# Kernel optimization log

Measured on AMD Instinct MI355X. Metric: run time of the kernel, lower is better.

Reference implementation:

```python
import jax, jax.numpy as jnp
import numpy as np

I_SIZE = 2048
O_SIZE = 2048
NUM_DOMAINS = 20
B, T = 16, 2048


def setup_inputs() -> dict:
    key = jax.random.key(0)
    k_x, k_w, k_d = jax.random.split(key, 3)
    x = jax.random.normal(k_x, (B, T, I_SIZE), dtype=jnp.float32)
    domain_id = jax.random.randint(k_d, (B,), 0, NUM_DOMAINS)
    # xavier_uniform over [num_domains, O*I]
    limit = float(np.sqrt(6.0 / (NUM_DOMAINS + O_SIZE * I_SIZE)))
    fc_weight = jax.random.uniform(k_w, (NUM_DOMAINS, O_SIZE * I_SIZE), dtype=jnp.float32, minval=-limit, maxval=limit)
    bias_weight = jnp.zeros((NUM_DOMAINS, O_SIZE), dtype=jnp.float32)
    return {"x": x, "domain_id": domain_id, "fc_weight": fc_weight, "bias_weight": bias_weight}


def reference(x, domain_id, fc_weight, bias_weight):
    # Gather per-sample weights: [B, I, O] (flat row reshaped as (I, O))
    W = fc_weight[domain_id].reshape(-1, I_SIZE, O_SIZE)
    b = bias_weight[domain_id]  # [B, O]
    # y = x @ W + b : [B, T, O]
    y = jnp.einsum('bti,bio->bto', x, W) + b[:, None, :]
    return y
```

## Files before the change

kernel.cpp:

```cpp
#include <hip/hip_runtime.h>
#include <hip/hip_bf16.h>
#include <stdint.h>

typedef __attribute__((ext_vector_type(4))) float  f32x4;
typedef __attribute__((ext_vector_type(8))) short  s16x8;
typedef __attribute__((ext_vector_type(4))) short  s16x4;

constexpr int I_SZ = 2048;
constexpr int O_SZ = 2048;
constexpr int T_SZ = 2048;
constexpr int B_MAX = 16;

constexpr size_t XT_ELEMS = (size_t)B_MAX * T_SZ * I_SZ;
constexpr size_t WT_ELEMS = (size_t)B_MAX * I_SZ * O_SZ;
constexpr size_t WS_NEEDED = (XT_ELEMS + WT_ELEMS) * sizeof(short);

__device__ __forceinline__ short f2bf(float f) {
    __hip_bfloat16 h = __float2bfloat16(f);
    return *reinterpret_cast<short*>(&h);
}

__device__ __forceinline__ void gload_lds16(const void* g, void* l) {
    __builtin_amdgcn_global_load_lds(
        (const __attribute__((address_space(1))) unsigned int*)g,
        (__attribute__((address_space(3))) unsigned int*)l, 16, 0, 0);
}

__global__ __launch_bounds__(256) void convA(const float* __restrict__ x,
                                             short* __restrict__ xt) {
    const int c = blockIdx.x * 256 + threadIdx.x;
    const int l  = c & 63;
    const int mi = (c >> 6) & 7;
    const int kt = (c >> 9) & 63;
    const int rest = c >> 15;
    const int mt = rest & 15, bz = rest >> 4;
    const int lr = l & 15, hi = l >> 4;
    const int m = mt * 128 + mi * 16 + lr;
    const float* src = x + ((size_t)(bz * T_SZ + m)) * I_SZ + kt * 32 + 4 * hi;
    f32x4 a = *reinterpret_cast<const f32x4*>(src);
    f32x4 b = *reinterpret_cast<const f32x4*>(src + 16);
    s16x8 h = { f2bf(a[0]), f2bf(a[1]), f2bf(a[2]), f2bf(a[3]),
                f2bf(b[0]), f2bf(b[1]), f2bf(b[2]), f2bf(b[3]) };
    *reinterpret_cast<s16x8*>(xt + (size_t)c * 8) = h;
}

__global__ __launch_bounds__(256) void convB(const float* __restrict__ fcw,
                                             const int* __restrict__ dom_id,
                                             short* __restrict__ wt) {
    const int c = blockIdx.x * 256 + threadIdx.x;
    const int l  = c & 63;
    const int ni = (c >> 6) & 7;
    const int kt = (c >> 9) & 63;
    const int rest = c >> 15;
    const int nt = rest & 15, bz = rest >> 4;
    const int lr = l & 15, hi = l >> 4;
    const int n = nt * 128 + ni * 16 + lr;
    const int dom = dom_id[bz];
    const float* src = fcw + (size_t)dom * ((size_t)I_SZ * O_SZ)
                           + (size_t)(kt * 32 + 4 * hi) * O_SZ + n;
    short h[8];
    #pragma unroll
    for (int j = 0; j < 4; ++j) {
        h[j]     = f2bf(src[(size_t)j * O_SZ]);
        h[4 + j] = f2bf(src[(size_t)(16 + j) * O_SZ]);
    }
    *reinterpret_cast<s16x8*>(wt + (size_t)c * 8) =
        *reinterpret_cast<s16x8*>(h);
}

__global__ __launch_bounds__(256, 2) void gemm_128x256(
        const short* __restrict__ xt, const short* __restrict__ wt,
        const float* __restrict__ bw, const int* __restrict__ dom_id,
        float* __restrict__ out) {
    __shared__ short As[3][8192];

    const int bid = blockIdx.x;
    const int swz = (bid & 7) * 256 + (bid >> 3);
    const int bz = swz >> 7;
    const int mb = (swz >> 3) & 15;
    const int nb = swz & 7;

    const int t = threadIdx.x;
    const int wv = t >> 6, l = t & 63;
    const int lr = l & 15, hi = l >> 4;
    const int nti  = wv >> 1;
    const int bsub = (wv & 1) * 4;

    const short* Abase = xt + (size_t)(bz * 16 + mb) * 64 * 4096;
    const short* Bp = wt + (size_t)((bz * 16 + nb * 2 + nti) * 64) * 4096
                         + bsub * 512 + l * 8;

    auto stageA = [&](int buf, int T) {
        #pragma unroll
        for (int r = 0; r < 4; ++r)
            gload_lds16(Abase + (size_t)(2 * T) * 4096 + r * 2048 + t * 8,
                        &As[buf][r * 2048 + t * 8]);
    };

    f32x4 acc[8][4] = {};

    stageA(0, 0);

    for (int T = 0; T < 32; ++T) {
        const int d = T % 3;

        s16x8 bq0[4], bq1[4];
        {
            const short* b0 = Bp + (size_t)(2 * T) * 4096;
            #pragma unroll
            for (int g = 0; g < 4; ++g)
                bq0[g] = *reinterpret_cast<const s16x8*>(b0 + g * 512);
            #pragma unroll
            for (int g = 0; g < 4; ++g)
                bq1[g] = *reinterpret_cast<const s16x8*>(b0 + 4096 + g * 512);
        }

        const int nT = (T + 1 < 32) ? T + 1 : 31;
        stageA((T + 1) % 3, nT);

        asm volatile("s_waitcnt vmcnt(4)" ::: "memory");
        asm volatile("s_barrier" ::: "memory");

        s16x8 af[8];
        #pragma unroll
        for (int f = 0; f < 8; ++f)
            af[f] = *reinterpret_cast<const s16x8*>(&As[d][f * 512 + l * 8]);
        __builtin_amdgcn_s_setprio(1);
        #pragma unroll
        for (int f = 0; f < 8; ++f)
            #pragma unroll
            for (int g = 0; g < 4; ++g)
                acc[f][g] = __builtin_amdgcn_mfma_f32_16x16x32_bf16(
                                af[f], bq0[g], acc[f][g], 0, 0, 0);
        __builtin_amdgcn_s_setprio(0);

        #pragma unroll
        for (int f = 0; f < 8; ++f)
            af[f] = *reinterpret_cast<const s16x8*>(&As[d][4096 + f * 512 + l * 8]);
        __builtin_amdgcn_s_setprio(1);
        #pragma unroll
        for (int f = 0; f < 8; ++f)
            #pragma unroll
            for (int g = 0; g < 4; ++g)
                acc[f][g] = __builtin_amdgcn_mfma_f32_16x16x32_bf16(
                                af[f], bq1[g], acc[f][g], 0, 0, 0);
        __builtin_amdgcn_s_setprio(0);
    }

    asm volatile("s_waitcnt vmcnt(0)" ::: "memory");

    const int dom = dom_id[bz];
    const int col0 = nb * 256 + wv * 64;
    float bias[4];
    #pragma unroll
    for (int g = 0; g < 4; ++g)
        bias[g] = bw[dom * O_SZ + col0 + g * 16 + lr];

    const size_t obase = ((size_t)bz * T_SZ + mb * 128) * O_SZ + col0;
    #pragma unroll
    for (int f = 0; f < 8; ++f) {
        #pragma unroll
        for (int r = 0; r < 4; ++r) {
            const int row = f * 16 + hi * 4 + r;
            float* orow = out + obase + (size_t)row * O_SZ;
            #pragma unroll
            for (int g = 0; g < 4; ++g)
                orow[g * 16 + lr] = acc[f][g][r] + bias[g];
        }
    }
}

constexpr int BM = 128, BN = 128, BK = 32;
constexpr int LDK = 40;
constexpr int NKT = I_SZ / BK;

__global__ __launch_bounds__(256) void dal_gemm(
    const float* __restrict__ x, const int* __restrict__ dom_id,
    const float* __restrict__ fcw, const float* __restrict__ bw,
    float* __restrict__ out)
{
    __shared__ short As[2][BM * LDK];
    __shared__ short Bs[2][BN * LDK];
    const int bz = blockIdx.z;
    const int m0 = blockIdx.y * BM, n0 = blockIdx.x * BN;
    const int dom = dom_id[bz];
    const float* Ag = x + ((size_t)bz * T_SZ + m0) * I_SZ;
    const float* Wg = fcw + (size_t)dom * ((size_t)I_SZ * O_SZ) + n0;
    const int t = threadIdx.x;
    const int am = t >> 3, ac = (t & 7) << 2;
    const int bk = (t >> 5) << 2, bn = (t & 31) << 2;
    const int wv = t >> 6, lane = t & 63;
    const int wr = (wv >> 1) << 6, wc = (wv & 1) << 6;
    const int hi = lane >> 4, lr = lane & 15;
    f32x4 acc[4][4] = {};
    f32x4 ra[4], rb[4];
    auto load_tile = [&](int kb) {
        #pragma unroll
        for (int p = 0; p < 4; ++p)
            ra[p] = *reinterpret_cast<const f32x4*>(Ag + (size_t)(am + 32 * p) * I_SZ + kb + ac);
        #pragma unroll
        for (int r = 0; r < 4; ++r)
            rb[r] = *reinterpret_cast<const f32x4*>(Wg + (size_t)(kb + bk + r) * O_SZ + bn);
    };
    auto store_tile = [&](int buf) {
        #pragma unroll
        for (int p = 0; p < 4; ++p) {
            s16x4 h = { f2bf(ra[p][0]), f2bf(ra[p][1]), f2bf(ra[p][2]), f2bf(ra[p][3]) };
            *reinterpret_cast<s16x4*>(&As[buf][(am + 32 * p) * LDK + ac]) = h;
        }
        #pragma unroll
        for (int i = 0; i < 4; ++i) {
            s16x4 h = { f2bf(rb[0][i]), f2bf(rb[1][i]), f2bf(rb[2][i]), f2bf(rb[3][i]) };
            *reinterpret_cast<s16x4*>(&Bs[buf][(bn + i) * LDK + bk]) = h;
        }
    };
    load_tile(0);
    store_tile(0);
    __syncthreads();
    for (int kt = 0; kt < NKT; ++kt) {
        const int cur = kt & 1;
        if (kt + 1 < NKT) load_tile((kt + 1) * BK);
        s16x8 af[4], bfr[4];
        #pragma unroll
        for (int im = 0; im < 4; ++im) {
            const short* p = &As[cur][(wr + im * 16 + lr) * LDK + 4 * hi];
            s16x4 lo = *reinterpret_cast<const s16x4*>(p);
            s16x4 hh = *reinterpret_cast<const s16x4*>(p + 16);
            af[im] = __builtin_shufflevector(lo, hh, 0, 1, 2, 3, 4, 5, 6, 7);
        }
        #pragma unroll
        for (int in = 0; in < 4; ++in) {
            const short* p = &Bs[cur][(wc + in * 16 + lr) * LDK + 4 * hi];
            s16x4 lo = *reinterpret_cast<const s16x4*>(p);
            s16x4 hh = *reinterpret_cast<const s16x4*>(p + 16);
            bfr[in] = __builtin_shufflevector(lo, hh, 0, 1, 2, 3, 4, 5, 6, 7);
        }
        #pragma unroll
        for (int im = 0; im < 4; ++im)
            #pragma unroll
            for (int in = 0; in < 4; ++in)
                acc[im][in] = __builtin_amdgcn_mfma_f32_16x16x32_bf16(
                                  af[im], bfr[in], acc[im][in], 0, 0, 0);
        if (kt + 1 < NKT) store_tile(cur ^ 1);
        __syncthreads();
    }
    float bias[4];
    #pragma unroll
    for (int in = 0; in < 4; ++in)
        bias[in] = bw[dom * O_SZ + n0 + wc + in * 16 + lr];
    const size_t obase = ((size_t)bz * T_SZ + m0) * O_SZ + n0;
    #pragma unroll
    for (int im = 0; im < 4; ++im) {
        #pragma unroll
        for (int r = 0; r < 4; ++r) {
            const int row = wr + im * 16 + hi * 4 + r;
            float* orow = out + obase + (size_t)row * O_SZ;
            #pragma unroll
            for (int in = 0; in < 4; ++in)
                orow[wc + in * 16 + lr] = acc[im][in][r] + bias[in];
        }
    }
}

extern "C" void kernel_launch(void* const* d_in, const int* in_sizes, int n_in,
                              void* d_out, int out_size, void* d_ws, size_t ws_size,
                              hipStream_t stream) {
    const float* x   = (const float*)d_in[0];
    const int*   dom = (const int*)d_in[1];
    const float* fcw = (const float*)d_in[2];
    const float* bw  = (const float*)d_in[3];
    float* out = (float*)d_out;
    const int B = in_sizes[1];

    if (ws_size >= WS_NEEDED && B == B_MAX) {
        short* xt = (short*)d_ws;
        short* wt = xt + XT_ELEMS;
        const int chunks = B * 16 * 64 * 512;
        convA<<<chunks / 256, 256, 0, stream>>>(x, xt);
        convB<<<chunks / 256, 256, 0, stream>>>(fcw, dom, wt);
        gemm_128x256<<<dim3(2048), dim3(256), 0, stream>>>(xt, wt, bw, dom, out);
    } else {
        dim3 grid(O_SZ / BN, T_SZ / BM, B);
        dal_gemm<<<grid, dim3(256), 0, stream>>>(x, dom, fcw, bw, out);
    }
}
```

Baseline: 404.0 us.

## Switch GEMM to 32x32x16 MFMA with repacked operands and deeper prefetch

Replaces the 16x16x32 bf16 MFMA tiles with 32x32x16 MFMA and changes the convA/convB pre-packing layouts to match the new fragment shape. It also restructures the main loop so B fragments for the next step load right after each half-phase and A tiles are staged two steps ahead in the triple buffer. The aim is fewer MFMA issues and LDS reads per FLOP, plus more overlap of global loads with compute. The epilogue is rewritten for the 32x32 accumulator layout, and the wait-count logic now depends on the new load ordering.

New measurement: 454.1 us. 12.4% more time.

```diff
diff --git a/kernel.cpp b/kernel.cpp
--- a/kernel.cpp
+++ b/kernel.cpp
@@ -2,9 +2,10 @@
 #include <hip/hip_bf16.h>
 #include <stdint.h>
 
-typedef __attribute__((ext_vector_type(4))) float  f32x4;
-typedef __attribute__((ext_vector_type(8))) short  s16x8;
-typedef __attribute__((ext_vector_type(4))) short  s16x4;
+typedef __attribute__((ext_vector_type(4)))  float f32x4;
+typedef __attribute__((ext_vector_type(16))) float f32x16;
+typedef __attribute__((ext_vector_type(8)))  short s16x8;
+typedef __attribute__((ext_vector_type(4)))  short s16x4;
 
 constexpr int I_SZ = 2048;
 constexpr int O_SZ = 2048;
@@ -29,16 +30,16 @@
 __global__ __launch_bounds__(256) void convA(const float* __restrict__ x,
                                              short* __restrict__ xt) {
     const int c = blockIdx.x * 256 + threadIdx.x;
-    const int l  = c & 63;
-    const int mi = (c >> 6) & 7;
-    const int kt = (c >> 9) & 63;
+    const int l   = c & 63;
+    const int sub = (c >> 6) & 3;
+    const int kt  = (c >> 8) & 127;
     const int rest = c >> 15;
     const int mt = rest & 15, bz = rest >> 4;
-    const int lr = l & 15, hi = l >> 4;
-    const int m = mt * 128 + mi * 16 + lr;
-    const float* src = x + ((size_t)(bz * T_SZ + m)) * I_SZ + kt * 32 + 4 * hi;
+    const int m = mt * 128 + sub * 32 + (l & 31);
+    const int kbase = kt * 16 + 4 * (l >> 5);
+    const float* src = x + ((size_t)(bz * T_SZ + m)) * I_SZ + kbase;
     f32x4 a = *reinterpret_cast<const f32x4*>(src);
-    f32x4 b = *reinterpret_cast<const f32x4*>(src + 16);
+    f32x4 b = *reinterpret_cast<const f32x4*>(src + 8);
     s16x8 h = { f2bf(a[0]), f2bf(a[1]), f2bf(a[2]), f2bf(a[3]),
                 f2bf(b[0]), f2bf(b[1]), f2bf(b[2]), f2bf(b[3]) };
     *reinterpret_cast<s16x8*>(xt + (size_t)c * 8) = h;
@@ -48,21 +49,21 @@
                                              const int* __restrict__ dom_id,
                                              short* __restrict__ wt) {
     const int c = blockIdx.x * 256 + threadIdx.x;
-    const int l  = c & 63;
-    const int ni = (c >> 6) & 7;
-    const int kt = (c >> 9) & 63;
+    const int l   = c & 63;
+    const int sub = (c >> 6) & 3;
+    const int kt  = (c >> 8) & 127;
     const int rest = c >> 15;
     const int nt = rest & 15, bz = rest >> 4;
-    const int lr = l & 15, hi = l >> 4;
-    const int n = nt * 128 + ni * 16 + lr;
+    const int n = nt * 128 + sub * 32 + (l & 31);
+    const int kbase = kt * 16 + 4 * (l >> 5);
     const int dom = dom_id[bz];
     const float* src = fcw + (size_t)dom * ((size_t)I_SZ * O_SZ)
-                           + (size_t)(kt * 32 + 4 * hi) * O_SZ + n;
+                           + (size_t)kbase * O_SZ + n;
     short h[8];
     #pragma unroll
     for (int j = 0; j < 4; ++j) {
         h[j]     = f2bf(src[(size_t)j * O_SZ]);
-        h[4 + j] = f2bf(src[(size_t)(16 + j) * O_SZ]);
+        h[4 + j] = f2bf(src[(size_t)(8 + j) * O_SZ]);
     }
     *reinterpret_cast<s16x8*>(wt + (size_t)c * 8) =
         *reinterpret_cast<s16x8*>(h);
@@ -82,90 +83,101 @@
 
     const int t = threadIdx.x;
     const int wv = t >> 6, l = t & 63;
-    const int lr = l & 15, hi = l >> 4;
-    const int nti  = wv >> 1;
-    const int bsub = (wv & 1) * 4;
-
-    const short* Abase = xt + (size_t)(bz * 16 + mb) * 64 * 4096;
-    const short* Bp = wt + (size_t)((bz * 16 + nb * 2 + nti) * 64) * 4096
+    const int lc = l & 31, lh = l >> 5;
+    const int nt128 = nb * 2 + (wv >> 1);
+    const int bsub  = 2 * (wv & 1);
+
+    const short* Abase = xt + (size_t)(bz * 16 + mb) * 262144;
+    const short* Bp = wt + (size_t)(bz * 16 + nt128) * 262144
                          + bsub * 512 + l * 8;
 
     auto stageA = [&](int buf, int T) {
         #pragma unroll
         for (int r = 0; r < 4; ++r)
-            gload_lds16(Abase + (size_t)(2 * T) * 4096 + r * 2048 + t * 8,
+            gload_lds16(Abase + (size_t)(4 * T + r) * 2048 + t * 8,
                         &As[buf][r * 2048 + t * 8]);
     };
 
-    f32x4 acc[8][4] = {};
+    f32x16 acc[4][2] = {};
+    s16x8 bqS0[4], bqS1[4];
+
+    auto loadS0 = [&](int T) {
+        #pragma unroll
+        for (int rr = 0; rr < 2; ++rr)
+            #pragma unroll
+            for (int g = 0; g < 2; ++g)
+                bqS0[rr * 2 + g] = *reinterpret_cast<const s16x8*>(
+                    Bp + (size_t)(4 * T + rr) * 2048 + g * 512);
+    };
+    auto loadS1 = [&](int T) {
+        #pragma unroll
+        for (int rr = 0; rr < 2; ++rr)
+            #pragma unroll
+            for (int g = 0; g < 2; ++g)
+                bqS1[rr * 2 + g] = *reinterpret_cast<const s16x8*>(
+                    Bp + (size_t)(4 * T + 2 + rr) * 2048 + g * 512);
+    };
+
+    auto phase = [&](int d, int r0, const s16x8* bq) {
+        #pragma unroll
+        for (int rr = 0; rr < 2; ++rr) {
+            const int r = r0 + rr;
+            s16x8 af[4];
+            #pragma unroll
+            for (int s = 0; s < 4; ++s)
+                af[s] = *reinterpret_cast<const s16x8*>(
+                            &As[d][r * 2048 + s * 512 + l * 8]);
+            __builtin_amdgcn_s_setprio(1);
+            #pragma unroll
+            for (int s = 0; s < 4; ++s)
+                #pragma unroll
+                for (int g = 0; g < 2; ++g)
+                    acc[s][g] = __builtin_amdgcn_mfma_f32_32x32x16_bf16(
+                                    af[s], bq[rr * 2 + g], acc[s][g], 0, 0, 0);
+            __builtin_amdgcn_s_setprio(0);
+        }
+    };
 
     stageA(0, 0);
+    loadS0(0);
+    loadS1(0);
+    stageA(1, 1);
 
     for (int T = 0; T < 32; ++T) {
         const int d = T % 3;
-
-        s16x8 bq0[4], bq1[4];
-        {
-            const short* b0 = Bp + (size_t)(2 * T) * 4096;
-            #pragma unroll
-            for (int g = 0; g < 4; ++g)
-                bq0[g] = *reinterpret_cast<const s16x8*>(b0 + g * 512);
-            #pragma unroll
-            for (int g = 0; g < 4; ++g)
-                bq1[g] = *reinterpret_cast<const s16x8*>(b0 + 4096 + g * 512);
-        }
-
         const int nT = (T + 1 < 32) ? T + 1 : 31;
-        stageA((T + 1) % 3, nT);
 
         asm volatile("s_waitcnt vmcnt(4)" ::: "memory");
         asm volatile("s_barrier" ::: "memory");
 
-        s16x8 af[8];
-        #pragma unroll
-        for (int f = 0; f < 8; ++f)
-            af[f] = *reinterpret_cast<const s16x8*>(&As[d][f * 512 + l * 8]);
-        __builtin_amdgcn_s_setprio(1);
-        #pragma unroll
-        for (int f = 0; f < 8; ++f)
-            #pragma unroll
-            for (int g = 0; g < 4; ++g)
-                acc[f][g] = __builtin_amdgcn_mfma_f32_16x16x32_bf16(
-                                af[f], bq0[g], acc[f][g], 0, 0, 0);
-        __builtin_amdgcn_s_setprio(0);
-
-        #pragma unroll
-        for (int f = 0; f < 8; ++f)
-            af[f] = *reinterpret_cast<const s16x8*>(&As[d][4096 + f * 512 + l * 8]);
-        __builtin_amdgcn_s_setprio(1);
-        #pragma unroll
-        for (int f = 0; f < 8; ++f)
-            #pragma unroll
-            for (int g = 0; g < 4; ++g)
-                acc[f][g] = __builtin_amdgcn_mfma_f32_16x16x32_bf16(
-                                af[f], bq1[g], acc[f][g], 0, 0, 0);
-        __builtin_amdgcn_s_setprio(0);
+        phase(d, 0, bqS0);
+        loadS0(nT);
+
+        phase(d, 2, bqS1);
+        loadS1(nT);
+        stageA((T + 2) % 3, (T + 2 < 32) ? T + 2 : 31);
     }
 
     asm volatile("s_waitcnt vmcnt(0)" ::: "memory");
 
     const int dom = dom_id[bz];
-    const int col0 = nb * 256 + wv * 64;
-    float bias[4];
-    #pragma unroll
-    for (int g = 0; g < 4; ++g)
-        bias[g] = bw[dom * O_SZ + col0 + g * 16 + lr];
+    const int col0 = nb * 256 + (wv >> 1) * 128 + (wv & 1) * 64;
+    float bias[2];
+    #pragma unroll
+    for (int g = 0; g < 2; ++g)
+        bias[g] = bw[dom * O_SZ + col0 + g * 32 + lc];
 
     const size_t obase = ((size_t)bz * T_SZ + mb * 128) * O_SZ + col0;
     #pragma unroll
-    for (int f = 0; f < 8; ++f) {
-        #pragma unroll
-        for (int r = 0; r < 4; ++r) {
-            const int row = f * 16 + hi * 4 + r;
-            float* orow = out + obase + (size_t)row * O_SZ;
-            #pragma unroll
-            for (int g = 0; g < 4; ++g)
-                orow[g * 16 + lr] = acc[f][g][r] + bias[g];
+    for (int s = 0; s < 4; ++s) {
+        #pragma unroll
+        for (int g = 0; g < 2; ++g) {
+            #pragma unroll
+            for (int r = 0; r < 16; ++r) {
+                const int row = s * 32 + (r & 3) + 8 * (r >> 2) + 4 * lh;
+                out[obase + (size_t)row * O_SZ + g * 32 + lc] =
+                    acc[s][g][r] + bias[g];
+            }
         }
     }
 }
@@ -275,7 +287,7 @@
     if (ws_size >= WS_NEEDED && B == B_MAX) {
         short* xt = (short*)d_ws;
         short* wt = xt + XT_ELEMS;
-        const int chunks = B * 16 * 64 * 512;
+        const int chunks = B * 16 * 128 * 4 * 64;
         convA<<<chunks / 256, 256, 0, stream>>>(x, xt);
         convB<<<chunks / 256, 256, 0, stream>>>(fcw, dom, wt);
         gemm_128x256<<<dim3(2048), dim3(256), 0, stream>>>(xt, wt, bw, dom, out);
```
